# Performance work log

Hardware: AMD Instinct MI355X
Metric: run time of the kernel (lower is better)

The kernel has to match this reference:

```python
import jax, jax.numpy as jnp
import numpy as np

IN_CH = 64
EMBED = 64
STRIDE = 1
F_SCALE = 2

def conv2d(x, w, b, pad, dil):
    y = jax.lax.conv_general_dilated(
        x, w, window_strides=(1, 1),
        padding=((pad, pad), (pad, pad)), rhs_dilation=(dil, dil),
        dimension_numbers=('NCHW', 'OIHW', 'NCHW'))
    return y + b[None, :, None, None]

def layer_norm_chw(x, eps=1e-5):
    # F.layer_norm(x, x.shape[-3:]) : normalize jointly over (C,H,W), no affine
    m = jnp.mean(x, axis=(1, 2, 3), keepdims=True)
    v = jnp.var(x, axis=(1, 2, 3), keepdims=True)
    return (x - m) / jnp.sqrt(v + eps)

def pixel_unshuffle_windows(x, f):
    # matches _pixel_unshuffle + rearrange 'b (f c) h w -> (b f) c h w'
    # (B,c,H,W) -> (B*f*f, c, H/f, W/f), window index k = dh*f + dw (outer)
    B, c, H, W = x.shape
    x = x.reshape(B, c, H // f, f, W // f, f)
    x = x.transpose(0, 3, 5, 1, 2, 4)  # B, dh, dw, c, h, w
    return x.reshape(B * f * f, c, H // f, W // f)

def get_attention(x, unet_output, wqk, convl_w, convl_b, f):
    B, c, H, W = x.shape
    xx = layer_norm_chw(x)
    qk_in = pixel_unshuffle_windows(xx, f)  # (B*f^2, c, sh, sw)
    v_in = pixel_unshuffle_windows(x, f)
    b2, _, sh, sw = qk_in.shape
    n = sh * sw
    qk = qk_in.transpose(0, 2, 3, 1).reshape(b2, n, c)  # (b h w) c ordering
    v = v_in.transpose(0, 2, 3, 1).reshape(b2, n, c)
    qk = qk @ wqk  # (b2, n, EMBED)
    qk = qk / (jnp.linalg.norm(qk, axis=-1, keepdims=True) + 1e-8)
    attn = (jnp.einsum('bne,bme->bnm', qk, qk) + 1.0) / jnp.sqrt(jnp.float32(EMBED))
    attn = jax.nn.softmax(attn, axis=-1)
    out = jnp.einsum('bnm,bmc->bnc', attn, v)
    # faithful raw reshape (as in torch code), not an inverse pixel shuffle
    out = out.reshape(B, -1, H, W)  # (B, c, H, W)
    out = jnp.concatenate([out, unet_output], axis=1)  # (B, 65, H, W)
    return conv2d(out, convl_w, convl_b, 0, 1)

def get_ff(x, c1w, c1b, c2w, c2b, c3w, c3b):
    x = jax.nn.relu(conv2d(x, c1w, c1b, STRIDE, STRIDE))
    x = jax.nn.relu(conv2d(x, c2w, c2b, STRIDE * 2, STRIDE * 2))
    return conv2d(x, c3w, c3b, 0, 1)

def setup_inputs() -> dict:
    key = jax.random.key(0)
    ks = jax.random.split(key, 12)
    B, C, H, W = 1, IN_CH, 128, 128
    s = 0.05
    return {
        'x': jax.random.normal(ks[0], (B, C, H, W), jnp.float32),
        'unet_output': jax.random.normal(ks[1], (B, 1, H, W), jnp.float32),
        'wqk': jax.random.normal(ks[2], (C, EMBED), jnp.float32) * 0.17,  # ~xavier gain 1.414
        'conv1_w': jax.random.normal(ks[3], (C, C, 3, 3), jnp.float32) * s,
        'conv1_b': jax.random.normal(ks[4], (C,), jnp.float32) * s,
        'conv2_w': jax.random.normal(ks[5], (C, C, 3, 3), jnp.float32) * s,
        'conv2_b': jax.random.normal(ks[6], (C,), jnp.float32) * s,
        'conv3_w': jax.random.normal(ks[7], (C, C, 1, 1), jnp.float32) * s,
        'conv3_b': jax.random.normal(ks[8], (C,), jnp.float32) * s,
        'convl_w': jax.random.normal(ks[9], (64, 65, 1, 1), jnp.float32) * s,
        'convl_b': jax.random.normal(ks[10], (64,), jnp.float32) * s,
    }

def reference(x, unet_output, wqk, conv1_w, conv1_b, conv2_w, conv2_b,
              conv3_w, conv3_b, convl_w, convl_b):
    f = F_SCALE * STRIDE
    attn_out = get_attention(x, unet_output, wqk, convl_w, convl_b, f)
    return x + get_ff(x + attn_out, conv1_w, conv1_b, conv2_w, conv2_b, conv3_w, conv3_b)
```

## Files before the change

kernel.cpp:

```cpp
#include <hip/hip_runtime.h>

typedef __bf16 bf16;
typedef bf16 bf16x8 __attribute__((ext_vector_type(8)));
typedef bf16 bf16x4 __attribute__((ext_vector_type(4)));
typedef float f32x4 __attribute__((ext_vector_type(4)));

#define MFMA16(a,b,c) __builtin_amdgcn_mfma_f32_16x16x32_bf16(a,b,c,0,0,0)

#define HW 16384
#define NQ 4096

constexpr size_t OFF_RED  = 0;
constexpr size_t OFF_Q    = 4096;
constexpr size_t OFF_VT   = OFF_Q  + (size_t)2097152;
constexpr size_t OFF_OP   = OFF_VT + (size_t)2097152;
constexpr size_t OFF_LP   = OFF_OP + (size_t)16777216;
constexpr size_t OFF_T    = OFF_LP + (size_t)524288;
constexpr size_t OFF_T2   = OFF_OP;
constexpr size_t OFF_T3   = OFF_OP + (size_t)2097152;
constexpr size_t OFF_W1   = OFF_T  + (size_t)2097152;
constexpr size_t OFF_W2   = OFF_W1 + 73728;
constexpr size_t OFF_W3   = OFF_W2 + 73728;
constexpr size_t OFF_WL   = OFF_W3 + 8192;

#define EC0 1.13314845f
#define EC1 0.141643556f
#define EC2 0.0088527222f
#define EC3 3.6886342e-4f

__global__ __launch_bounds__(256) void k_red1w(const float* __restrict__ x, float* __restrict__ red,
                                               const float* __restrict__ w1, const float* __restrict__ w2,
                                               const float* __restrict__ w3, const float* __restrict__ wlc,
                                               bf16* __restrict__ W1, bf16* __restrict__ W2,
                                               bf16* __restrict__ W3, bf16* __restrict__ WLb) {
    int t = threadIdx.x, bx = blockIdx.x;
    if (bx >= 256) {
        int g = (bx - 256) * 256 + t;
        if (g < 36864) {
            int tap = g >> 12, co = (g >> 6) & 63, ci = g & 63;
            W1[g] = (bf16)w1[(co*64 + ci)*9 + tap];
        } else if (g < 73728) {
            int d = g - 36864;
            int tap = d >> 12, co = (d >> 6) & 63, ci = d & 63;
            W2[d] = (bf16)w2[(co*64 + ci)*9 + tap];
        } else if (g < 77824) {
            int d = g - 73728;
            W3[d] = (bf16)w3[d];
        } else if (g < 81920) {
            int d = g - 77824;
            WLb[d] = (bf16)wlc[(d >> 6)*65 + (d & 63)];
        }
        return;
    }
    float s = 0.f;
    const float* base = x + (size_t)bx*4096;
    #pragma unroll
    for (int k = 0; k < 4; ++k) {
        float4 v = *(const float4*)(base + k*1024 + t*4);
        s += v.x + v.y + v.z + v.w;
    }
    __shared__ float rs[256];
    rs[t] = s; __syncthreads();
    for (int off = 128; off; off >>= 1) {
        if (t < off) rs[t] += rs[t+off];
        __syncthreads();
    }
    if (t == 0) red[bx] = rs[0];
}

__global__ __launch_bounds__(256) void k_qv(const float* __restrict__ x, const float* __restrict__ wqk,
                                            const float* __restrict__ red,
                                            bf16* __restrict__ Q, bf16* __restrict__ Vt) {
    int t = threadIdx.x, bx = blockIdx.x;
    int y = bx >> 2, x0 = (bx & 3) * 32;
    __shared__ float xs[32][65];
    __shared__ float wl[4096];
    __shared__ float rs[256];
    __shared__ float vv[64];

    rs[t] = red[t];
    __syncthreads();
    for (int off = 128; off; off >>= 1) {
        if (t < off) rs[t] += rs[t+off];
        __syncthreads();
    }

    {
        int c = t >> 2, seg = t & 3;
        const float4* xp = (const float4*)(x + (size_t)c*HW + y*128 + x0 + seg*8);
        float f[8];
        float4 v0 = xp[0], v1 = xp[1];
        f[0]=v0.x; f[1]=v0.y; f[2]=v0.z; f[3]=v0.w;
        f[4]=v1.x; f[5]=v1.y; f[6]=v1.z; f[7]=v1.w;
        #pragma unroll
        for (int k = 0; k < 8; ++k) xs[seg*8 + k][c] = f[k];
        int dh = y & 1;
        int base_n = (y >> 1)*64 + ((x0 + seg*8) >> 1);
        bf16* vte = Vt + ((size_t)((dh*2 + 0)*64 + c))*NQ + base_n;
        bf16* vto = Vt + ((size_t)((dh*2 + 1)*64 + c))*NQ + base_n;
        #pragma unroll
        for (int j = 0; j < 4; ++j) { vte[j] = (bf16)f[2*j]; vto[j] = (bf16)f[2*j+1]; }
    }
    {
        const float4* wp = (const float4*)wqk;
        #pragma unroll
        for (int k = 0; k < 4; ++k) {
            float4 v = wp[t*4 + k];
            wl[t*16 + k*4 + 0] = v.x; wl[t*16 + k*4 + 1] = v.y;
            wl[t*16 + k*4 + 2] = v.z; wl[t*16 + k*4 + 3] = v.w;
        }
    }
    __syncthreads();
    if (t < 64) {
        float cs = 0.f;
        for (int c = 0; c < 64; ++c) cs += wl[c*64 + t];
        vv[t] = rs[0] * (1.f/1048576.f) * cs;
    }
    __syncthreads();

    int p = t >> 3, eg = t & 7;
    float acc[8];
    #pragma unroll
    for (int k = 0; k < 8; ++k) acc[k] = 0.f;
    for (int c = 0; c < 64; ++c) {
        float xv = xs[p][c];
        const float* wr = &wl[c*64 + eg*8];
        #pragma unroll
        for (int k = 0; k < 8; ++k) acc[k] += xv * wr[k];
    }
    #pragma unroll
    for (int k = 0; k < 8; ++k) acc[k] -= vv[eg*8 + k];
    float ss = 0.f;
    #pragma unroll
    for (int k = 0; k < 8; ++k) ss += acc[k]*acc[k];
    ss += __shfl_xor(ss, 1);
    ss += __shfl_xor(ss, 2);
    ss += __shfl_xor(ss, 4);
    float inv = 1.f / (sqrtf(ss) + 1e-8f);

    int xp2 = x0 + p;
    int b2 = (y & 1)*2 + (xp2 & 1);
    int nidx = (y >> 1)*64 + (xp2 >> 1);
    bf16x8 qv;
    #pragma unroll
    for (int k = 0; k < 8; ++k) qv[k] = (bf16)(acc[k]*inv);
    *(bf16x8*)(Q + ((size_t)b2*NQ + nidx)*64 + eg*8) = qv;
}

__global__ __launch_bounds__(256, 2) void k_attn(const bf16* __restrict__ Q, const bf16* __restrict__ Vt,
                                                 bf16* __restrict__ Opart, float* __restrict__ lpart) {
    int bx = blockIdx.x;
    int b2 = bx & 3;
    int jq = (bx >> 2) & 7;
    int it = bx >> 5;
    int tid = threadIdx.x;
    int w = tid >> 6, lane = tid & 63, q = lane >> 4, l15 = lane & 15;
    int ibase = it*256 + w*64;

    const bf16* Qb = Q  + (size_t)b2*NQ*64;
    const bf16* Vb = Vt + (size_t)b2*64*NQ;

    bf16x8 aq[4][2];
    #pragma unroll
    for (int nt = 0; nt < 4; ++nt) {
        const bf16* p = Qb + (size_t)(ibase + nt*16 + l15)*64 + q*8;
        aq[nt][0] = *(const bf16x8*)p;
        aq[nt][1] = *(const bf16x8*)(p + 32);
    }
    bf16x8 ones;
    #pragma unroll
    for (int k = 0; k < 8; ++k) ones[k] = (bf16)1.0f;

    f32x4 o[4][4];
    f32x4 ol[4];
    #pragma unroll
    for (int mt = 0; mt < 4; ++mt) {
        ol[mt] = (f32x4){0.f,0.f,0.f,0.f};
        #pragma unroll
        for (int n = 0; n < 4; ++n) o[mt][n] = (f32x4){0.f,0.f,0.f,0.f};
    }

    __shared__ __align__(16) bf16 Qs[64][72];
    __shared__ __align__(16) bf16 Vs[64][72];
    __shared__ __align__(16) bf16 plds[4][64][72];

    int srow = tid >> 2, scol = (tid & 3) * 16;
    int j0 = jq * 512;
    for (int itj = 0; itj < 8; ++itj) {
        int jt = j0 + itj*64;
        __syncthreads();
        {
            const bf16* qsrc = Qb + (size_t)(jt + srow)*64 + scol;
            *(bf16x8*)&Qs[srow][scol]     = *(const bf16x8*)qsrc;
            *(bf16x8*)&Qs[srow][scol + 8] = *(const bf16x8*)(qsrc + 8);
            const bf16* vsrc = Vb + (size_t)srow*NQ + jt + scol;
            *(bf16x8*)&Vs[srow][scol]     = *(const bf16x8*)vsrc;
            *(bf16x8*)&Vs[srow][scol + 8] = *(const bf16x8*)(vsrc + 8);
        }
        __syncthreads();

        f32x4 z = (f32x4){0.f,0.f,0.f,0.f};
        #pragma unroll
        for (int mtj = 0; mtj < 4; ++mtj) {
            bf16x8 a0 = *(const bf16x8*)&Qs[mtj*16 + l15][q*8];
            bf16x8 a1 = *(const bf16x8*)&Qs[mtj*16 + l15][32 + q*8];
            #pragma unroll
            for (int nti = 0; nti < 4; ++nti) {
                f32x4 s = MFMA16(a0, aq[nti][0], z);
                s = MFMA16(a1, aq[nti][1], s);
                bf16x4 pk;
                #pragma unroll
                for (int r = 0; r < 4; ++r) {
                    float sv = s[r];
                    pk[r] = (bf16)fmaf(fmaf(fmaf(EC3, sv, EC2), sv, EC1), sv, EC0);
                }
                *(bf16x4*)&plds[w][nti*16 + l15][mtj*16 + q*4] = pk;
            }
        }
        #pragma unroll
        for (int kj = 0; kj < 2; ++kj) {
            bf16x8 ap[4], bv[4];
            #pragma unroll
            for (int mt = 0; mt < 4; ++mt)
                ap[mt] = *(const bf16x8*)&plds[w][mt*16 + l15][kj*32 + q*8];
            #pragma unroll
            for (int nc = 0; nc < 4; ++nc)
                bv[nc] = *(const bf16x8*)&Vs[nc*16 + l15][kj*32 + q*8];
            #pragma unroll
            for (int mt = 0; mt < 4; ++mt) {
                ol[mt] = MFMA16(ap[mt], ones, ol[mt]);
                #pragma unroll
                for (int nc = 0; nc < 4; ++nc)
                    o[mt][nc] = MFMA16(ap[mt], bv[nc], o[mt][nc]);
            }
        }
    }

    #pragma unroll
    for (int mt = 0; mt < 4; ++mt) {
        #pragma unroll
        for (int r = 0; r < 4; ++r) {
            int gr = b2*NQ + ibase + mt*16 + q*4 + r;
            bf16* orow = Opart + ((size_t)jq*16384 + gr)*64;
            #pragma unroll
            for (int nc = 0; nc < 4; ++nc) orow[nc*16 + l15] = (bf16)o[mt][nc][r];
            if (l15 == 0) lpart[(size_t)jq*16384 + gr] = ol[mt][r];
        }
    }
}

__global__ __launch_bounds__(256) void k_convl(const bf16* __restrict__ Op, const float* __restrict__ lp,
                                               const float* __restrict__ unet, const float* __restrict__ x,
                                               const bf16* __restrict__ WLb, const float* __restrict__ wl,
                                               const float* __restrict__ bl, bf16* __restrict__ T) {
    int t = threadIdx.x, bx = blockIdx.x;
    int p0 = bx * 64;
    __shared__ __align__(16) bf16 As[64][72];
    {
        int ci = t >> 2, seg = t & 3;
        int gr = ((ci >> 4) << 12) + ((ci & 15) << 8) + bx;
        float lsum = 0.f;
        #pragma unroll
        for (int p = 0; p < 8; ++p) lsum += lp[p*16384 + gr];
        float linv = 1.f / lsum;
        float acc[16];
        #pragma unroll
        for (int k = 0; k < 16; ++k) acc[k] = 0.f;
        #pragma unroll
        for (int p = 0; p < 8; ++p) {
            const bf16* src = Op + ((size_t)p*16384 + gr)*64 + seg*16;
            bf16x8 v0 = *(const bf16x8*)src;
            bf16x8 v1 = *(const bf16x8*)(src + 8);
            #pragma unroll
            for (int k = 0; k < 8; ++k) { acc[k] += (float)v0[k]; acc[8+k] += (float)v1[k]; }
        }
        #pragma unroll
        for (int k = 0; k < 16; ++k) As[seg*16 + k][ci] = (bf16)(acc[k] * linv);
    }
    __syncthreads();

    int w = t >> 6, lane = t & 63, q = lane >> 4, l15 = lane & 15;
    int co = w*16 + l15;
    const bf16* wp = WLb + co*64 + q*8;
    bf16x8 b0 = *(const bf16x8*)wp;
    bf16x8 b1 = *(const bf16x8*)(wp + 32);
    f32x4 z = (f32x4){0.f,0.f,0.f,0.f};
    f32x4 o[4];
    #pragma unroll
    for (int mt = 0; mt < 4; ++mt) {
        bf16x8 a0 = *(const bf16x8*)&As[mt*16 + l15][q*8];
        bf16x8 a1 = *(const bf16x8*)&As[mt*16 + l15][32 + q*8];
        f32x4 s = MFMA16(a0, b0, z);
        o[mt] = MFMA16(a1, b1, s);
    }
    float wlu = wl[co*65 + 64];
    float bias = bl[co];
    #pragma unroll
    for (int mt = 0; mt < 4; ++mt) {
        int pb = p0 + mt*16 + q*4;
        float4 un  = *(const float4*)(unet + pb);
        float4 xs4 = *(const float4*)(x + (size_t)co*HW + pb);
        float xv[4] = {xs4.x, xs4.y, xs4.z, xs4.w};
        float uv[4] = {un.x, un.y, un.z, un.w};
        #pragma unroll
        for (int r = 0; r < 4; ++r) {
            float v = o[mt][r] + uv[r]*wlu + bias + xv[r];
            T[(size_t)(pb + r)*64 + co] = (bf16)v;
        }
    }
}

__global__ __launch_bounds__(256) void k_conv3x3(const bf16* __restrict__ IN, const bf16* __restrict__ WT,
                                                 const float* __restrict__ B, bf16* __restrict__ OUT,
                                                 int dil) {
    int tid = threadIdx.x, bx = blockIdx.x;
    int y = bx >> 3, xh = (bx >> 2) & 1, coq = bx & 3;
    int w = tid >> 6, lane = tid & 63, q = lane >> 4, l15 = lane & 15;
    int xb = xh*64 + w*16;

    __shared__ __align__(16) bf16 wsl[9][16][72];
    for (int i = tid; i < 1152; i += 256) {
        int tap = i >> 7, rem = i & 127, co = rem >> 3, k8 = (rem & 7) * 8;
        *(bf16x8*)&wsl[tap][co][k8] =
            *(const bf16x8*)(WT + (((size_t)(tap*64 + coq*16 + co)) << 6) + k8);
    }
    __syncthreads();

    f32x4 o = (f32x4){0.f,0.f,0.f,0.f};
    #pragma unroll
    for (int ky = 0; ky < 3; ++ky) {
        int yy = y + (ky - 1)*dil;
        bool yok = (yy >= 0) && (yy < 128);
        #pragma unroll
        for (int kx = 0; kx < 3; ++kx) {
            int xx = xb + l15 + (kx - 1)*dil;
            bool ok = yok && (xx >= 0) && (xx < 128);
            bf16x8 alo = {}, ahi = {};
            if (ok) {
                const bf16* ip = IN + (size_t)(yy*128 + xx)*64 + q*8;
                alo = *(const bf16x8*)ip;
                ahi = *(const bf16x8*)(ip + 32);
            }
            int tap = ky*3 + kx;
            bf16x8 blo = *(const bf16x8*)&wsl[tap][l15][q*8];
            bf16x8 bhi = *(const bf16x8*)&wsl[tap][l15][32 + q*8];
            o = MFMA16(alo, blo, o);
            o = MFMA16(ahi, bhi, o);
        }
    }
    int co = coq*16 + l15;
    float bias = B[co];
    #pragma unroll
    for (int r = 0; r < 4; ++r) {
        float v = fmaxf(o[r] + bias, 0.f);
        OUT[(size_t)(y*128 + xb + q*4 + r)*64 + co] = (bf16)v;
    }
}

__global__ __launch_bounds__(256) void k_conv3(const bf16* __restrict__ T3, const bf16* __restrict__ W3,
                                               const float* __restrict__ b3, const float* __restrict__ x,
                                               float* __restrict__ out) {
    int tid = threadIdx.x, bx = blockIdx.x;
    int pg = bx >> 1, coh = bx & 1;
    int w = tid >> 6, lane = tid & 63, q = lane >> 4, l15 = lane & 15;
    int p0 = pg*64 + w*16;
    const bf16* bp = T3 + (size_t)(p0 + l15)*64 + q*8;
    bf16x8 blo = *(const bf16x8*)bp;
    bf16x8 bhi = *(const bf16x8*)(bp + 32);
    f32x4 z = (f32x4){0.f,0.f,0.f,0.f};
    f32x4 o[2];
    #pragma unroll
    for (int mt = 0; mt < 2; ++mt) {
        const bf16* ap = W3 + (size_t)(coh*32 + mt*16 + l15)*64 + q*8;
        bf16x8 alo = *(const bf16x8*)ap;
        bf16x8 ahi = *(const bf16x8*)(ap + 32);
        f32x4 s = MFMA16(alo, blo, z);
        o[mt] = MFMA16(ahi, bhi, s);
    }
    #pragma unroll
    for (int mt = 0; mt < 2; ++mt) {
        #pragma unroll
        for (int r = 0; r < 4; ++r) {
            int co = coh*32 + mt*16 + q*4 + r;
            size_t idx = (size_t)co*HW + p0 + l15;
            out[idx] = x[idx] + b3[co] + o[mt][r];
        }
    }
}

extern "C" void kernel_launch(void* const* d_in, const int* in_sizes, int n_in,
                              void* d_out, int out_size, void* d_ws, size_t ws_size,
                              hipStream_t stream) {
    (void)in_sizes; (void)n_in; (void)out_size; (void)ws_size;
    const float* x    = (const float*)d_in[0];
    const float* unet = (const float*)d_in[1];
    const float* wqk  = (const float*)d_in[2];
    const float* c1w  = (const float*)d_in[3];
    const float* c1b  = (const float*)d_in[4];
    const float* c2w  = (const float*)d_in[5];
    const float* c2b  = (const float*)d_in[6];
    const float* c3w  = (const float*)d_in[7];
    const float* c3b  = (const float*)d_in[8];
    const float* clw  = (const float*)d_in[9];
    const float* clb  = (const float*)d_in[10];
    float* out = (float*)d_out;

    char* ws = (char*)d_ws;
    float* red   = (float*)(ws + OFF_RED);
    bf16*  Q     = (bf16*)(ws + OFF_Q);
    bf16*  Vt    = (bf16*)(ws + OFF_VT);
    bf16*  Opart = (bf16*)(ws + OFF_OP);
    float* lpart = (float*)(ws + OFF_LP);
    bf16*  T     = (bf16*)(ws + OFF_T);
    bf16*  T2    = (bf16*)(ws + OFF_T2);
    bf16*  T3    = (bf16*)(ws + OFF_T3);
    bf16*  W1    = (bf16*)(ws + OFF_W1);
    bf16*  W2    = (bf16*)(ws + OFF_W2);
    bf16*  W3    = (bf16*)(ws + OFF_W3);
    bf16*  WLb   = (bf16*)(ws + OFF_WL);

    k_red1w<<<dim3(576), dim3(256), 0, stream>>>(x, red, c1w, c2w, c3w, clw, W1, W2, W3, WLb);
    k_qv<<<dim3(512),    dim3(256), 0, stream>>>(x, wqk, red, Q, Vt);
    k_attn<<<dim3(512),  dim3(256), 0, stream>>>(Q, Vt, Opart, lpart);
    k_convl<<<dim3(256), dim3(256), 0, stream>>>(Opart, lpart, unet, x, WLb, clw, clb, T);
    k_conv3x3<<<dim3(1024), dim3(256), 0, stream>>>(T,  W1, c1b, T2, 1);
    k_conv3x3<<<dim3(1024), dim3(256), 0, stream>>>(T2, W2, c2b, T3, 2);
    k_conv3<<<dim3(512), dim3(256), 0, stream>>>(T3, W3, c3b, x, out);
}
```

Measured before the change: 143.0 us.

## Replace quadratic attention with first-order linearized attention via two small GEMMs

Because q is L2-normalized, each attention logit (q·k+1)/8 is bounded. The code therefore approximates exp with its first-order expansion, which turns softmax(QQᵀ)V into Q·(QᵀV) plus row-sum terms. k_attn and the partial-output reduction are replaced by two kernels. k_gemm1 builds a per-window 80x80 matrix of KᵀV, column sums and row sums, split over 4 chunks, and k_gemm2 multiplies Q by it and normalizes. This removes the O(N²) score computation and the large Opart/lpart traffic, and k_qv now also writes a transposed Q. The trade-off is extra approximation error from dropping the higher-order terms of exp, plus only 16 and 64 blocks in the new kernels, so the GPU is under-occupied.

Result: slower. 151.3 us (+5.8%).

```diff
diff --git a/kernel.cpp b/kernel.cpp
--- a/kernel.cpp
+++ b/kernel.cpp
@@ -2,7 +2,6 @@
 
 typedef __bf16 bf16;
 typedef bf16 bf16x8 __attribute__((ext_vector_type(8)));
-typedef bf16 bf16x4 __attribute__((ext_vector_type(4)));
 typedef float f32x4 __attribute__((ext_vector_type(4)));
 
 #define MFMA16(a,b,c) __builtin_amdgcn_mfma_f32_16x16x32_bf16(a,b,c,0,0,0)
@@ -12,21 +11,17 @@
 
 constexpr size_t OFF_RED  = 0;
 constexpr size_t OFF_Q    = 4096;
-constexpr size_t OFF_VT   = OFF_Q  + (size_t)2097152;
-constexpr size_t OFF_OP   = OFF_VT + (size_t)2097152;
-constexpr size_t OFF_LP   = OFF_OP + (size_t)16777216;
-constexpr size_t OFF_T    = OFF_LP + (size_t)524288;
-constexpr size_t OFF_T2   = OFF_OP;
-constexpr size_t OFF_T3   = OFF_OP + (size_t)2097152;
-constexpr size_t OFF_W1   = OFF_T  + (size_t)2097152;
+constexpr size_t OFF_QT   = OFF_Q  + (size_t)2097152;
+constexpr size_t OFF_VT   = OFF_QT + (size_t)2097152;
+constexpr size_t OFF_MP   = OFF_VT + (size_t)2097152;
+constexpr size_t OFF_AT   = OFF_MP + (size_t)524288;
+constexpr size_t OFF_T    = OFF_AT + (size_t)2097152;
+constexpr size_t OFF_T2   = OFF_AT;
+constexpr size_t OFF_T3   = OFF_T  + (size_t)2097152;
+constexpr size_t OFF_W1   = OFF_T3 + (size_t)2097152;
 constexpr size_t OFF_W2   = OFF_W1 + 73728;
 constexpr size_t OFF_W3   = OFF_W2 + 73728;
 constexpr size_t OFF_WL   = OFF_W3 + 8192;
-
-#define EC0 1.13314845f
-#define EC1 0.141643556f
-#define EC2 0.0088527222f
-#define EC3 3.6886342e-4f
 
 __global__ __launch_bounds__(256) void k_red1w(const float* __restrict__ x, float* __restrict__ red,
                                                const float* __restrict__ w1, const float* __restrict__ w2,
@@ -70,13 +65,15 @@
 
 __global__ __launch_bounds__(256) void k_qv(const float* __restrict__ x, const float* __restrict__ wqk,
                                             const float* __restrict__ red,
-                                            bf16* __restrict__ Q, bf16* __restrict__ Vt) {
+                                            bf16* __restrict__ Q, bf16* __restrict__ Qt,
+                                            bf16* __restrict__ Vt) {
     int t = threadIdx.x, bx = blockIdx.x;
     int y = bx >> 2, x0 = (bx & 3) * 32;
     __shared__ float xs[32][65];
     __shared__ float wl[4096];
     __shared__ float rs[256];
     __shared__ float vv[64];
+    __shared__ bf16 qts[64][34];
 
     rs[t] = red[t];
     __syncthreads();
@@ -145,111 +142,113 @@
     #pragma unroll
     for (int k = 0; k < 8; ++k) qv[k] = (bf16)(acc[k]*inv);
     *(bf16x8*)(Q + ((size_t)b2*NQ + nidx)*64 + eg*8) = qv;
-}
-
-__global__ __launch_bounds__(256, 2) void k_attn(const bf16* __restrict__ Q, const bf16* __restrict__ Vt,
-                                                 bf16* __restrict__ Opart, float* __restrict__ lpart) {
+    #pragma unroll
+    for (int k = 0; k < 8; ++k) qts[eg*8 + k][p] = qv[k];
+    __syncthreads();
+
+    {
+        int e = t >> 2, par = (t >> 1) & 1, seg2 = t & 1;
+        int b2w = (y & 1)*2 + par;
+        int nbase = (y >> 1)*64 + (x0 >> 1) + seg2*8;
+        bf16x8 qt;
+        #pragma unroll
+        for (int j = 0; j < 8; ++j) qt[j] = qts[e][par + 2*(seg2*8 + j)];
+        *(bf16x8*)(Qt + ((size_t)b2w*64 + e)*NQ + nbase) = qt;
+    }
+}
+
+__global__ __launch_bounds__(320) void k_gemm1(const bf16* __restrict__ Vt, const bf16* __restrict__ Qt,
+                                               float* __restrict__ MP) {
     int bx = blockIdx.x;
-    int b2 = bx & 3;
-    int jq = (bx >> 2) & 7;
-    int it = bx >> 5;
-    int tid = threadIdx.x;
-    int w = tid >> 6, lane = tid & 63, q = lane >> 4, l15 = lane & 15;
-    int ibase = it*256 + w*64;
-
-    const bf16* Qb = Q  + (size_t)b2*NQ*64;
-    const bf16* Vb = Vt + (size_t)b2*64*NQ;
-
-    bf16x8 aq[4][2];
-    #pragma unroll
-    for (int nt = 0; nt < 4; ++nt) {
-        const bf16* p = Qb + (size_t)(ibase + nt*16 + l15)*64 + q*8;
-        aq[nt][0] = *(const bf16x8*)p;
-        aq[nt][1] = *(const bf16x8*)(p + 32);
-    }
-    bf16x8 ones;
-    #pragma unroll
-    for (int k = 0; k < 8; ++k) ones[k] = (bf16)1.0f;
-
-    f32x4 o[4][4];
-    f32x4 ol[4];
+    int b2 = bx & 3, kc = bx >> 2;
+    int tid = threadIdx.x, w = tid >> 6, lane = tid & 63, q = lane >> 4, l15 = lane & 15;
+    const bf16* Vb  = Vt + (size_t)b2*64*NQ;
+    const bf16* Qtb = Qt + (size_t)b2*64*NQ;
+    bf16x8 onesfrag = {};
+    if (l15 == 0) {
+        #pragma unroll
+        for (int k = 0; k < 8; ++k) onesfrag[k] = (bf16)1.0f;
+    }
+    f32x4 acc[5];
+    #pragma unroll
+    for (int nt = 0; nt < 5; ++nt) acc[nt] = (f32x4){0.f,0.f,0.f,0.f};
+
+    int k0 = kc*1024 + q*8;
+    for (int it = 0; it < 32; ++it) {
+        int kk = k0 + it*32;
+        bf16x8 a;
+        if (w < 4) a = *(const bf16x8*)(Vb + (size_t)(w*16 + l15)*NQ + kk);
+        else       a = onesfrag;
+        bf16x8 b[5];
+        #pragma unroll
+        for (int nt = 0; nt < 4; ++nt) b[nt] = *(const bf16x8*)(Qtb + (size_t)(nt*16 + l15)*NQ + kk);
+        b[4] = onesfrag;
+        #pragma unroll
+        for (int nt = 0; nt < 5; ++nt) acc[nt] = MFMA16(a, b[nt], acc[nt]);
+    }
+    float* mp = MP + (size_t)bx*6400;
+    #pragma unroll
+    for (int nt = 0; nt < 5; ++nt)
+        #pragma unroll
+        for (int r = 0; r < 4; ++r)
+            mp[(w*16 + q*4 + r)*80 + nt*16 + l15] = acc[nt][r];
+}
+
+__global__ __launch_bounds__(256) void k_gemm2(const bf16* __restrict__ Q, const float* __restrict__ MP,
+                                               bf16* __restrict__ attn) {
+    int bx = blockIdx.x;
+    int b2 = bx & 3, nh = bx >> 2;
+    int tid = threadIdx.x, w = tid >> 6, lane = tid & 63, q = lane >> 4, l15 = lane & 15;
+    __shared__ __align__(16) bf16 Ms[80][80];
+    for (int i = tid; i < 6400; i += 256) {
+        float s = MP[(size_t)b2*6400 + i] + MP[(size_t)(b2+4)*6400 + i]
+                + MP[(size_t)(b2+8)*6400 + i] + MP[(size_t)(b2+12)*6400 + i];
+        int rr = i / 80;
+        Ms[rr][i - rr*80] = (bf16)s;
+    }
+    __syncthreads();
+
+    const bf16* Qb = Q + ((size_t)b2*NQ + nh*256 + w*64)*64;
+    f32x4 acc[4][5];
+    #pragma unroll
+    for (int mt = 0; mt < 4; ++mt)
+        #pragma unroll
+        for (int ct = 0; ct < 5; ++ct) acc[mt][ct] = (f32x4){0.f,0.f,0.f,0.f};
+
+    #pragma unroll
+    for (int kt = 0; kt < 2; ++kt) {
+        bf16x8 bfr[5];
+        #pragma unroll
+        for (int ct = 0; ct < 5; ++ct) bfr[ct] = *(const bf16x8*)&Ms[ct*16 + l15][kt*32 + q*8];
+        #pragma unroll
+        for (int mt = 0; mt < 4; ++mt) {
+            bf16x8 a = *(const bf16x8*)(Qb + (size_t)(mt*16 + l15)*64 + kt*32 + q*8);
+            #pragma unroll
+            for (int ct = 0; ct < 5; ++ct) acc[mt][ct] = MFMA16(a, bfr[ct], acc[mt][ct]);
+        }
+    }
+    float c0v[4];
+    #pragma unroll
+    for (int ct = 0; ct < 4; ++ct) c0v[ct] = (float)Ms[ct*16 + l15][64];
+
+    bf16* arow = attn + (size_t)(b2*16 + nh)*HW + w*64*64;
     #pragma unroll
     for (int mt = 0; mt < 4; ++mt) {
-        ol[mt] = (f32x4){0.f,0.f,0.f,0.f};
-        #pragma unroll
-        for (int n = 0; n < 4; ++n) o[mt][n] = (f32x4){0.f,0.f,0.f,0.f};
-    }
-
-    __shared__ __align__(16) bf16 Qs[64][72];
-    __shared__ __align__(16) bf16 Vs[64][72];
-    __shared__ __align__(16) bf16 plds[4][64][72];
-
-    int srow = tid >> 2, scol = (tid & 3) * 16;
-    int j0 = jq * 512;
-    for (int itj = 0; itj < 8; ++itj) {
-        int jt = j0 + itj*64;
-        __syncthreads();
-        {
-            const bf16* qsrc = Qb + (size_t)(jt + srow)*64 + scol;
-            *(bf16x8*)&Qs[srow][scol]     = *(const bf16x8*)qsrc;
-            *(bf16x8*)&Qs[srow][scol + 8] = *(const bf16x8*)(qsrc + 8);
-            const bf16* vsrc = Vb + (size_t)srow*NQ + jt + scol;
-            *(bf16x8*)&Vs[srow][scol]     = *(const bf16x8*)vsrc;
-            *(bf16x8*)&Vs[srow][scol + 8] = *(const bf16x8*)(vsrc + 8);
-        }
-        __syncthreads();
-
-        f32x4 z = (f32x4){0.f,0.f,0.f,0.f};
-        #pragma unroll
-        for (int mtj = 0; mtj < 4; ++mtj) {
-            bf16x8 a0 = *(const bf16x8*)&Qs[mtj*16 + l15][q*8];
-            bf16x8 a1 = *(const bf16x8*)&Qs[mtj*16 + l15][32 + q*8];
+        #pragma unroll
+        for (int r = 0; r < 4; ++r) {
+            float ldot = __shfl(acc[mt][4][r], lane & 48);
+            float rl = 1.0f / fmaf(ldot, 0.125f, 4096.0f);
+            int rr = mt*16 + q*4 + r;
             #pragma unroll
-            for (int nti = 0; nti < 4; ++nti) {
-                f32x4 s = MFMA16(a0, aq[nti][0], z);
-                s = MFMA16(a1, aq[nti][1], s);
-                bf16x4 pk;
-                #pragma unroll
-                for (int r = 0; r < 4; ++r) {
-                    float sv = s[r];
-                    pk[r] = (bf16)fmaf(fmaf(fmaf(EC3, sv, EC2), sv, EC1), sv, EC0);
-                }
-                *(bf16x4*)&plds[w][nti*16 + l15][mtj*16 + q*4] = pk;
+            for (int ct = 0; ct < 4; ++ct) {
+                float v = fmaf(acc[mt][ct][r], 0.125f, c0v[ct]) * rl;
+                arow[rr*64 + ct*16 + l15] = (bf16)v;
             }
         }
-        #pragma unroll
-        for (int kj = 0; kj < 2; ++kj) {
-            bf16x8 ap[4], bv[4];
-            #pragma unroll
-            for (int mt = 0; mt < 4; ++mt)
-                ap[mt] = *(const bf16x8*)&plds[w][mt*16 + l15][kj*32 + q*8];
-            #pragma unroll
-            for (int nc = 0; nc < 4; ++nc)
-                bv[nc] = *(const bf16x8*)&Vs[nc*16 + l15][kj*32 + q*8];
-            #pragma unroll
-            for (int mt = 0; mt < 4; ++mt) {
-                ol[mt] = MFMA16(ap[mt], ones, ol[mt]);
-                #pragma unroll
-                for (int nc = 0; nc < 4; ++nc)
-                    o[mt][nc] = MFMA16(ap[mt], bv[nc], o[mt][nc]);
-            }
-        }
-    }
-
-    #pragma unroll
-    for (int mt = 0; mt < 4; ++mt) {
-        #pragma unroll
-        for (int r = 0; r < 4; ++r) {
-            int gr = b2*NQ + ibase + mt*16 + q*4 + r;
-            bf16* orow = Opart + ((size_t)jq*16384 + gr)*64;
-            #pragma unroll
-            for (int nc = 0; nc < 4; ++nc) orow[nc*16 + l15] = (bf16)o[mt][nc][r];
-            if (l15 == 0) lpart[(size_t)jq*16384 + gr] = ol[mt][r];
-        }
-    }
-}
-
-__global__ __launch_bounds__(256) void k_convl(const bf16* __restrict__ Op, const float* __restrict__ lp,
+    }
+}
+
+__global__ __launch_bounds__(256) void k_convl(const bf16* __restrict__ attn,
                                                const float* __restrict__ unet, const float* __restrict__ x,
                                                const bf16* __restrict__ WLb, const float* __restrict__ wl,
                                                const float* __restrict__ bl, bf16* __restrict__ T) {
@@ -258,24 +257,11 @@
     __shared__ __align__(16) bf16 As[64][72];
     {
         int ci = t >> 2, seg = t & 3;
-        int gr = ((ci >> 4) << 12) + ((ci & 15) << 8) + bx;
-        float lsum = 0.f;
-        #pragma unroll
-        for (int p = 0; p < 8; ++p) lsum += lp[p*16384 + gr];
-        float linv = 1.f / lsum;
-        float acc[16];
-        #pragma unroll
-        for (int k = 0; k < 16; ++k) acc[k] = 0.f;
-        #pragma unroll
-        for (int p = 0; p < 8; ++p) {
-            const bf16* src = Op + ((size_t)p*16384 + gr)*64 + seg*16;
-            bf16x8 v0 = *(const bf16x8*)src;
-            bf16x8 v1 = *(const bf16x8*)(src + 8);
-            #pragma unroll
-            for (int k = 0; k < 8; ++k) { acc[k] += (float)v0[k]; acc[8+k] += (float)v1[k]; }
-        }
-        #pragma unroll
-        for (int k = 0; k < 16; ++k) As[seg*16 + k][ci] = (bf16)(acc[k] * linv);
+        const bf16* src = attn + (size_t)ci*HW + p0 + seg*16;
+        bf16x8 v0 = *(const bf16x8*)src;
+        bf16x8 v1 = *(const bf16x8*)(src + 8);
+        #pragma unroll
+        for (int k = 0; k < 8; ++k) { As[seg*16 + k][ci] = v0[k]; As[seg*16 + 8 + k][ci] = v1[k]; }
     }
     __syncthreads();
 
@@ -408,9 +394,10 @@
     char* ws = (char*)d_ws;
     float* red   = (float*)(ws + OFF_RED);
     bf16*  Q     = (bf16*)(ws + OFF_Q);
+    bf16*  Qt    = (bf16*)(ws + OFF_QT);
     bf16*  Vt    = (bf16*)(ws + OFF_VT);
-    bf16*  Opart = (bf16*)(ws + OFF_OP);
-    float* lpart = (float*)(ws + OFF_LP);
+    float* MP    = (float*)(ws + OFF_MP);
+    bf16*  attn  = (bf16*)(ws + OFF_AT);
     bf16*  T     = (bf16*)(ws + OFF_T);
     bf16*  T2    = (bf16*)(ws + OFF_T2);
     bf16*  T3    = (bf16*)(ws + OFF_T3);
@@ -420,9 +407,10 @@
     bf16*  WLb   = (bf16*)(ws + OFF_WL);
 
     k_red1w<<<dim3(576), dim3(256), 0, stream>>>(x, red, c1w, c2w, c3w, clw, W1, W2, W3, WLb);
-    k_qv<<<dim3(512),    dim3(256), 0, stream>>>(x, wqk, red, Q, Vt);
-    k_attn<<<dim3(512),  dim3(256), 0, stream>>>(Q, Vt, Opart, lpart);
-    k_convl<<<dim3(256), dim3(256), 0, stream>>>(Opart, lpart, unet, x, WLb, clw, clb, T);
+    k_qv<<<dim3(512),    dim3(256), 0, stream>>>(x, wqk, red, Q, Qt, Vt);
+    k_gemm1<<<dim3(16),  dim3(320), 0, stream>>>(Vt, Qt, MP);
+    k_gemm2<<<dim3(64),  dim3(256), 0, stream>>>(Q, MP, attn);
+    k_convl<<<dim3(256), dim3(256), 0, stream>>>(attn, unet, x, WLb, clw, clb, T);
     k_conv3x3<<<dim3(1024), dim3(256), 0, stream>>>(T,  W1, c1b, T2, 1);
     k_conv3x3<<<dim3(1024), dim3(256), 0, stream>>>(T2, W2, c2b, T3, 2);
     k_conv3<<<dim3(512), dim3(256), 0, stream>>>(T3, W3, c3b, x, out);
```
